# Kernel optimization log

Hardware: AMD Instinct MI355X
Metric: run time of the kernel (lower is better)

Reference implementation:

```python
import jax, jax.numpy as jnp
import numpy as np

V, T, E, H, B, S = 50000, 45, 256, 512, 32, 256


def setup_inputs() -> dict:
    key = jax.random.key(0)
    ks = jax.random.split(key, 14)
    s = 0.05
    return dict(
        x=jax.random.randint(ks[0], (B, S), 0, V),
        tags=jax.random.randint(ks[1], (B, S), 0, T),
        mask=jnp.ones((B, S), dtype=bool),
        emb=jax.random.normal(ks[2], (V, E), jnp.float32),
        Wih_f=jax.random.normal(ks[3], (4 * H, E), jnp.float32) * s,
        Whh_f=jax.random.normal(ks[4], (4 * H, H), jnp.float32) * s,
        bih_f=jnp.zeros((4 * H,), jnp.float32),
        bhh_f=jnp.zeros((4 * H,), jnp.float32),
        Wih_b=jax.random.normal(ks[5], (4 * H, E), jnp.float32) * s,
        Whh_b=jax.random.normal(ks[6], (4 * H, H), jnp.float32) * s,
        bih_b=jnp.zeros((4 * H,), jnp.float32),
        bhh_b=jnp.zeros((4 * H,), jnp.float32),
        Wout=jax.random.normal(ks[7], (T, 2 * H), jnp.float32) * s,
        bout=jnp.zeros((T,), jnp.float32),
        start=jax.random.normal(ks[8], (T,), jnp.float32) * 0.1,
        end=jax.random.normal(ks[9], (T,), jnp.float32) * 0.1,
        trans=jax.random.normal(ks[10], (T, T), jnp.float32) * 0.1,
    )


def _lstm_dir(xp, Whh, reverse):
    # xp: [S, B, 4H] precomputed input projection + biases; gate order i,f,g,o (torch)
    Bn = xp.shape[1]
    Hn = Whh.shape[1]
    def step(carry, g_in):
        h, c = carry
        g = g_in + h @ Whh.T
        i, f, gg, o = jnp.split(g, 4, axis=-1)
        c = jax.nn.sigmoid(f) * c + jax.nn.sigmoid(i) * jnp.tanh(gg)
        h = jax.nn.sigmoid(o) * jnp.tanh(c)
        return (h, c), h
    init = (jnp.zeros((Bn, Hn), xp.dtype), jnp.zeros((Bn, Hn), xp.dtype))
    _, hs = jax.lax.scan(step, init, xp, reverse=reverse)
    return hs  # [S, B, H]


def _crf_nll(emissions, tags, mask, start, end, trans):
    # emissions: [B, S, T]; neg mean log-likelihood (torchcrf, reduction='mean')
    mf = mask.astype(emissions.dtype)
    em_tag = jnp.take_along_axis(emissions, tags[:, :, None], axis=2)[:, :, 0]  # [B,S]
    num = start[tags[:, 0]] + em_tag[:, 0]
    num = num + ((trans[tags[:, :-1], tags[:, 1:]] + em_tag[:, 1:]) * mf[:, 1:]).sum(1)
    seq_ends = mf.sum(1).astype(tags.dtype) - 1
    last_tags = jnp.take_along_axis(tags, seq_ends[:, None], axis=1)[:, 0]
    num = num + end[last_tags]
    def denom_step(alpha, inp):
        em_t, m_t = inp  # [B,T], [B]
        nxt = jax.nn.logsumexp(alpha[:, :, None] + trans[None, :, :] + em_t[:, None, :], axis=1)
        return jnp.where(m_t[:, None] > 0, nxt, alpha), None
    alpha0 = start[None, :] + emissions[:, 0]
    em_rest = emissions.transpose(1, 0, 2)[1:]  # [S-1, B, T]
    alpha, _ = jax.lax.scan(denom_step, alpha0, (em_rest, mf.T[1:]))
    logZ = jax.nn.logsumexp(alpha + end[None, :], axis=1)
    return -(num - logZ).mean()


def reference(x, tags, mask, emb, Wih_f, Whh_f, bih_f, bhh_f,
              Wih_b, Whh_b, bih_b, bhh_b, Wout, bout, start, end, trans):
    embeds = emb[x]                      # [B, S, E]
    xs = embeds.transpose(1, 0, 2)       # [S, B, E]
    xp_f = jnp.einsum('sbe,ge->sbg', xs, Wih_f) + bih_f + bhh_f
    hs_f = _lstm_dir(xp_f, Whh_f, False)
    xp_b = jnp.einsum('sbe,ge->sbg', xs, Wih_b) + bih_b + bhh_b
    hs_b = _lstm_dir(xp_b, Whh_b, True)
    hcat = jnp.concatenate([hs_f, hs_b], axis=-1)          # [S, B, 2H]
    emissions = jnp.einsum('sbh,th->sbt', hcat, Wout) + bout
    emissions = emissions.transpose(1, 0, 2)                # [B, S, T]
    return _crf_nll(emissions, tags, mask, start, end, trans)
```

## Files before the change

### kernel.cpp

```cpp
#include <hip/hip_runtime.h>
#include <stdint.h>

#define S_LEN 256
#define B_N 32
#define H_N 512
#define E_N 256
#define T_N 45
#define G4H 2048

typedef unsigned short u16;
typedef unsigned int u32;
typedef u16 u16x8 __attribute__((ext_vector_type(8)));
typedef u16 u16x4 __attribute__((ext_vector_type(4)));
typedef u32 u32x4 __attribute__((ext_vector_type(4)));
typedef u32 u32x2 __attribute__((ext_vector_type(2)));
typedef __bf16 bf16x8 __attribute__((ext_vector_type(8)));
typedef float f32x4 __attribute__((ext_vector_type(4)));
typedef unsigned long long u64;

#define OFF_ATOK  256ull
#define OFF_WIHF  (OFF_ATOK + 4194304ull)
#define OFF_WIHB  (OFF_WIHF + 1048576ull)
#define OFF_WHHF  (OFF_WIHB + 1048576ull)
#define OFF_WHHB  (OFF_WHHF + 2097152ull)
#define OFF_WOUT  (OFF_WHHB + 2097152ull)
#define OFF_BSF   (OFF_WOUT + 98304ull)
#define OFF_BSB   (OFF_BSF + 8192ull)
#define OFF_XPF   (OFF_BSB + 8192ull)
#define OFF_XPB   (OFF_XPF + 33554432ull)
#define OFF_HSF   (OFF_XPB + 33554432ull)
#define OFF_HSB   (OFF_HSF + 8421376ull)
#define OFF_EM    (OFF_HSB + 8421376ull)

__device__ __forceinline__ u16 f2bf(float f) {
  union { float f; unsigned u; } v; v.f = f;
  unsigned r = v.u + 0x7FFFu + ((v.u >> 16) & 1u);
  return (u16)(r >> 16);
}
__device__ __forceinline__ float bf2f(u16 b) {
  union { unsigned u; float f; } v; v.u = ((unsigned)b) << 16;
  return v.f;
}
__device__ __forceinline__ bf16x8 ld8(const u16* p) {
  u16x8 v = *reinterpret_cast<const u16x8*>(p);
  return __builtin_bit_cast(bf16x8, v);
}
__device__ __forceinline__ void st_h8cc(u16* p, u16x4 v) {
  __hip_atomic_store(reinterpret_cast<u64*>(p), __builtin_bit_cast(u64, v),
                     __ATOMIC_RELAXED, __HIP_MEMORY_SCOPE_AGENT);
}
__device__ __forceinline__ u32x4 ld16cc(const u16* p) {
  u32x4 r;
  asm volatile("global_load_dwordx4 %0, %1, off sc1"
               : "=v"(r) : "v"(p) : "memory");
  return r;
}
__device__ __forceinline__ u32x2 ld8cc(const u16* p) {
  u32x2 r;
  asm volatile("global_load_dwordx2 %0, %1, off sc1"
               : "=v"(r) : "v"(p) : "memory");
  return r;
}
__device__ __forceinline__ void st2cc(u16* p, u32 v) {
  asm volatile("global_store_short %0, %1, off sc1"
               :: "v"(p), "v"(v) : "memory");
}
__device__ __forceinline__ f32x4 mfma16(bf16x8 a, bf16x8 b, f32x4 c) {
  return __builtin_amdgcn_mfma_f32_16x16x32_bf16(a, b, c, 0, 0, 0);
}
__device__ __forceinline__ float sigm(float x) { return 1.f / (1.f + __expf(-x)); }
__device__ __forceinline__ float tanhf_(float x) {
  float ax = fabsf(x);
  float e = __expf(-2.f * ax);
  float t = 1.f - 2.f * e / (1.f + e);
  return (x < 0.f) ? -t : t;
}
__device__ __forceinline__ float wredmax(float v) {
  #pragma unroll
  for (int m = 1; m < 64; m <<= 1) v = fmaxf(v, __shfl_xor(v, m));
  return v;
}
__device__ __forceinline__ float wredsum(float v) {
  #pragma unroll
  for (int m = 1; m < 64; m <<= 1) v += __shfl_xor(v, m);
  return v;
}

__global__ void k_castAW(const int* __restrict__ x, const float* __restrict__ emb,
                         u16* __restrict__ atok,
                         const float* __restrict__ WihF, const float* __restrict__ WihB,
                         const float* __restrict__ WhhF, const float* __restrict__ WhhB,
                         const float* __restrict__ Wout,
                         const float* __restrict__ bihF, const float* __restrict__ bhhF,
                         const float* __restrict__ bihB, const float* __restrict__ bhhB,
                         u16* wihf, u16* wihb, u16* whhf, u16* whhb, u16* woutp,
                         float* bsf, float* bsb, u16* hsf, u16* hsb) {
  int bid = blockIdx.x;
  if (bid < 1024) {
    int idx = bid * 256 + threadIdx.x;
    int t = idx >> 5;
    int e0 = (idx & 31) << 3;
    int s = t >> 5, b = t & 31;
    int xid = x[b * S_LEN + s];
    const float4* p = reinterpret_cast<const float4*>(emb + (size_t)xid * E_N + e0);
    float4 lo = p[0], hi = p[1];
    u16x8 o;
    o[0] = f2bf(lo.x); o[1] = f2bf(lo.y); o[2] = f2bf(lo.z); o[3] = f2bf(lo.w);
    o[4] = f2bf(hi.x); o[5] = f2bf(hi.y); o[6] = f2bf(hi.z); o[7] = f2bf(hi.w);
    *reinterpret_cast<u16x8*>(atok + (size_t)t * E_N + e0) = o;
    return;
  }
  int i = (bid - 1024) * 256 + threadIdx.x;
  if (i < 524288) { wihf[i] = f2bf(WihF[i]); return; }
  i -= 524288;
  if (i < 524288) { wihb[i] = f2bf(WihB[i]); return; }
  i -= 524288;
  if (i < 1048576) { whhf[i] = f2bf(WhhF[i]); return; }
  i -= 1048576;
  if (i < 1048576) { whhb[i] = f2bf(WhhB[i]); return; }
  i -= 1048576;
  if (i < 49152) {
    int n = i >> 10, k = i & 1023;
    woutp[i] = (n < T_N) ? f2bf(Wout[n * 1024 + k]) : (u16)0;
    return;
  }
  i -= 49152;
  if (i < 2048) { bsf[i] = bihF[i] + bhhF[i]; return; }
  i -= 2048;
  if (i < 2048) { bsb[i] = bihB[i] + bhhB[i]; return; }
  i -= 2048;
  if (i < 16384) { hsf[i] = 0; return; }
  i -= 16384;
  if (i < 16384) { hsb[(size_t)256 * 16384 + i] = 0; return; }
}

__global__ __launch_bounds__(128, 1) void k_fused(
    const u16* __restrict__ whhF, const u16* __restrict__ whhB,
    const u16* __restrict__ atok,
    const u16* __restrict__ wihF, const u16* __restrict__ wihB,
    const float* __restrict__ bsF, const float* __restrict__ bsB,
    u16* __restrict__ xpF, u16* __restrict__ xpB,
    u16* __restrict__ hsF, u16* __restrict__ hsB) {
  if (blockIdx.x >= 64) {
    int j = (int)blockIdx.x - 64;
    int dir = j & 1, idx = j >> 1;
    int tIdx = idx >> 4, gIdx = idx & 15;
    if (dir) tIdx = 127 - tIdx;
    const int wave = threadIdx.x >> 6, lane = threadIdx.x & 63;
    const int lr = lane & 15, lh = lane >> 4;
    const int t0 = tIdx * 64;
    const int g0 = gIdx * 128 + wave * 64;
    const u16* wih = dir ? wihB : wihF;
    const float* bs = dir ? bsB : bsF;
    u16* xp = dir ? xpB : xpF;
    f32x4 acc[4][4] = {};
    for (int kk = 0; kk < 8; ++kk) {
      int e = kk * 32 + lh * 8;
      bf16x8 a[4], bfr[4];
      #pragma unroll
      for (int mi = 0; mi < 4; ++mi) a[mi] = ld8(atok + (size_t)(t0 + 16 * mi + lr) * E_N + e);
      #pragma unroll
      for (int ni = 0; ni < 4; ++ni) bfr[ni] = ld8(wih + (size_t)(g0 + 16 * ni + lr) * E_N + e);
      #pragma unroll
      for (int mi = 0; mi < 4; ++mi)
        #pragma unroll
        for (int ni = 0; ni < 4; ++ni) acc[mi][ni] = mfma16(a[mi], bfr[ni], acc[mi][ni]);
    }
    #pragma unroll
    for (int ni = 0; ni < 4; ++ni) {
      int g = g0 + 16 * ni + lr;
      float bsv = bs[g];
      #pragma unroll
      for (int mi = 0; mi < 4; ++mi)
        #pragma unroll
        for (int r = 0; r < 4; ++r) {
          int t = t0 + 16 * mi + 4 * lh + r;
          st2cc(xp + (size_t)t * G4H + g, (u32)f2bf(acc[mi][ni][r] + bsv));
        }
    }
    return;
  }
  const int dir = blockIdx.x >> 5;
  const int w = blockIdx.x & 31;
  const int nt = threadIdx.x >> 6;
  const int lane = threadIdx.x & 63;
  const int lr = lane & 15, lh = lane >> 4;
  const u16* whh = dir ? whhB : whhF;
  const u16* xp = dir ? xpB : xpF;
  u16* hs = dir ? hsB : hsF;

  bf16x8 A[4][16];
  #pragma unroll
  for (int mt = 0; mt < 4; ++mt) {
    const u16* base = whh + (size_t)(mt * 512 + 16 * w + lr) * H_N + lh * 8;
    #pragma unroll
    for (int kk = 0; kk < 16; ++kk) A[mt][kk] = ld8(base + kk * 32);
  }
  const int b = nt * 16 + lr;
  const int j0 = 16 * w + 4 * lh;
  float cst[4] = {0.f, 0.f, 0.f, 0.f};

  for (int t = 0; t < S_LEN; ++t) {
    const int s = dir ? (S_LEN - 1 - t) : t;
    const int slot_r = dir ? (s + 1) : s;
    const int slot_w = dir ? s : (s + 1);

    u32x2 xqr[4];
    const u16* xpt = xp + ((size_t)(s * B_N + b)) * G4H + j0;
    #pragma unroll
    for (int mt = 0; mt < 4; ++mt) xqr[mt] = ld8cc(xpt + mt * 512);

    const u16* hp = hs + ((size_t)slot_r * B_N + b) * H_N + lh * 8;
    u32x4 raw[16];
    #pragma unroll
    for (int kk = 0; kk < 16; ++kk) raw[kk] = ld16cc(hp + kk * 32);
    asm volatile("s_waitcnt vmcnt(0)" ::: "memory");
    __builtin_amdgcn_sched_barrier(0);
    u32 pend = 0;
    #pragma unroll
    for (int kk = 0; kk < 16; ++kk)
      if (raw[kk][0] == 0xFFFFFFFFu || raw[kk][2] == 0xFFFFFFFFu) pend |= (1u << kk);
    while (__builtin_amdgcn_ballot_w64(pend != 0u)) {
      __builtin_amdgcn_s_sleep(1);
      #pragma unroll
      for (int kk = 0; kk < 16; ++kk)
        if (pend & (1u << kk)) raw[kk] = ld16cc(hp + kk * 32);
      asm volatile("s_waitcnt vmcnt(0)" ::: "memory");
      __builtin_amdgcn_sched_barrier(0);
      u32 np = 0;
      #pragma unroll
      for (int kk = 0; kk < 16; ++kk)
        if ((pend & (1u << kk)) &&
            (raw[kk][0] == 0xFFFFFFFFu || raw[kk][2] == 0xFFFFFFFFu)) np |= (1u << kk);
      pend = np;
    }

    f32x4 acc[4] = {};
    #pragma unroll
    for (int kk = 0; kk < 16; ++kk) {
      bf16x8 Bf = __builtin_bit_cast(bf16x8, raw[kk]);
      #pragma unroll
      for (int mt = 0; mt < 4; ++mt) acc[mt] = mfma16(A[mt][kk], Bf, acc[mt]);
    }

    for (;;) {
      u32 xbad = 0;
      #pragma unroll
      for (int mt = 0; mt < 4; ++mt) {
        #pragma unroll
        for (int d = 0; d < 2; ++d) {
          u32 wv = xqr[mt][d];
          xbad |= ((wv & 0xFFFFu) == 0xFFFFu) | ((wv >> 16) == 0xFFFFu);
        }
      }
      if (!__builtin_amdgcn_ballot_w64(xbad != 0u)) break;
      __builtin_amdgcn_s_sleep(1);
      #pragma unroll
      for (int mt = 0; mt < 4; ++mt) xqr[mt] = ld8cc(xpt + mt * 512);
      asm volatile("s_waitcnt vmcnt(0)" ::: "memory");
      __builtin_amdgcn_sched_barrier(0);
    }

    u16x4 hv;
    #pragma unroll
    for (int r = 0; r < 4; ++r) {
      u32 w0 = xqr[0][r >> 1], w1 = xqr[1][r >> 1], w2 = xqr[2][r >> 1], w3 = xqr[3][r >> 1];
      u16 x0 = (r & 1) ? (u16)(w0 >> 16) : (u16)(w0 & 0xFFFFu);
      u16 x1 = (r & 1) ? (u16)(w1 >> 16) : (u16)(w1 & 0xFFFFu);
      u16 x2 = (r & 1) ? (u16)(w2 >> 16) : (u16)(w2 & 0xFFFFu);
      u16 x3 = (r & 1) ? (u16)(w3 >> 16) : (u16)(w3 & 0xFFFFu);
      float gi = acc[0][r] + bf2f(x0);
      float gf = acc[1][r] + bf2f(x1);
      float gg = acc[2][r] + bf2f(x2);
      float go = acc[3][r] + bf2f(x3);
      float c = sigm(gf) * cst[r] + sigm(gi) * tanhf_(gg);
      cst[r] = c;
      hv[r] = f2bf(sigm(go) * tanhf_(c));
    }
    st_h8cc(hs + ((size_t)slot_w * B_N + b) * H_N + j0, hv);
  }
}

__global__ __launch_bounds__(256) void k_gemm_em(
    const u16* __restrict__ hsF, const u16* __restrict__ hsB,
    const u16* __restrict__ woutp, const float* __restrict__ bout, float* __restrict__ em) {
  const int wave = threadIdx.x >> 6, lane = threadIdx.x & 63;
  const int lr = lane & 15, lh = lane >> 4;
  const int t0 = blockIdx.x * 64 + wave * 16;
  f32x4 acc[3] = {};
  for (int kk = 0; kk < 32; ++kk) {
    int k = kk * 32 + lh * 8;
    int t = t0 + lr;
    int s = t >> 5, bt = t & 31;
    const u16* ap = (kk < 16) ? (hsF + ((size_t)(s + 1) * B_N + bt) * H_N + k)
                              : (hsB + ((size_t)s * B_N + bt) * H_N + (k - 512));
    bf16x8 a = ld8(ap);
    #pragma unroll
    for (int ni = 0; ni < 3; ++ni) {
      bf16x8 bb = ld8(woutp + (size_t)(16 * ni + lr) * 1024 + k);
      acc[ni] = mfma16(a, bb, acc[ni]);
    }
  }
  #pragma unroll
  for (int ni = 0; ni < 3; ++ni) {
    int tag = 16 * ni + lr;
    float bo = (tag < T_N) ? bout[tag] : 0.f;
    #pragma unroll
    for (int r = 0; r < 4; ++r) {
      int t = t0 + 4 * lh + r;
      em[(size_t)t * 48 + tag] = acc[ni][r] + bo;
    }
  }
}

__global__ __launch_bounds__(64) void k_crf(
    const float* __restrict__ em, const int* __restrict__ tags,
    const float* __restrict__ start, const float* __restrict__ endv,
    const float* __restrict__ trans, float* __restrict__ out) {
  __shared__ float tl[T_N * T_N + 32];
  const int b = blockIdx.x;
  const int lane = threadIdx.x;
  for (int i = lane; i < T_N * T_N + 32; i += 64)
    tl[i] = (i < T_N * T_N) ? trans[i] : 0.f;
  __syncthreads();
  float acur = (lane < T_N) ? (start[lane] + em[(size_t)b * 48 + lane]) : -1e30f;
  float emv_next = (lane < 48) ? em[((size_t)(1 * B_N + b)) * 48 + lane] : 0.f;
  for (int s = 1; s < S_LEN; ++s) {
    float shift = wredmax(acur);
    float emv = emv_next;
    if (s < S_LEN - 1)
      emv_next = (lane < 48) ? em[((size_t)((s + 1) * B_N + b)) * 48 + lane] : 0.f;
    float s0 = 0.f, s1 = 0.f, s2 = 0.f;
    #pragma unroll
    for (int t = 0; t < T_N; t += 3) {
      s0 += __expf(__shfl(acur, t)     + tl[t * T_N + lane]       - shift);
      s1 += __expf(__shfl(acur, t + 1) + tl[(t + 1) * T_N + lane] - shift);
      s2 += __expf(__shfl(acur, t + 2) + tl[(t + 2) * T_N + lane] - shift);
    }
    acur = (lane < T_N) ? (shift + __logf(s0 + s1 + s2) + emv) : -1e30f;
  }
  float z = (lane < T_N) ? (acur + endv[lane]) : -1e30f;
  float m = wredmax(z);
  float sum = wredsum((lane < T_N) ? __expf(z - m) : 0.f);
  float logZ = m + __logf(sum);
  float np = 0.f;
  #pragma unroll
  for (int q = 0; q < 4; ++q) {
    int s = 1 + lane * 4 + q;
    if (s < S_LEN) {
      int tp = tags[b * S_LEN + s - 1], tc = tags[b * S_LEN + s];
      np += tl[tp * T_N + tc] + em[((size_t)s * B_N + b) * 48 + tc];
    }
  }
  np = wredsum(np);
  if (lane == 0) {
    int tg0 = tags[b * S_LEN], tgL = tags[b * S_LEN + S_LEN - 1];
    float num = start[tg0] + em[(size_t)b * 48 + tg0] + np + endv[tgL];
    atomicAdd(out, -(num - logZ) / (float)B_N);
  }
}

extern "C" void kernel_launch(void* const* d_in, const int* in_sizes, int n_in,
                              void* d_out, int out_size, void* d_ws, size_t ws_size,
                              hipStream_t stream) {
  const int* x = (const int*)d_in[0];
  const int* tags = (const int*)d_in[1];
  const float* emb = (const float*)d_in[3];
  const float* WihF = (const float*)d_in[4];
  const float* WhhF = (const float*)d_in[5];
  const float* bihF = (const float*)d_in[6];
  const float* bhhF = (const float*)d_in[7];
  const float* WihB = (const float*)d_in[8];
  const float* WhhB = (const float*)d_in[9];
  const float* bihB = (const float*)d_in[10];
  const float* bhhB = (const float*)d_in[11];
  const float* Wout = (const float*)d_in[12];
  const float* bout = (const float*)d_in[13];
  const float* start = (const float*)d_in[14];
  const float* endv = (const float*)d_in[15];
  const float* trans = (const float*)d_in[16];
  float* out = (float*)d_out;
  char* ws = (char*)d_ws;

  u16* atok = (u16*)(ws + OFF_ATOK);
  u16* wihf = (u16*)(ws + OFF_WIHF);
  u16* wihb = (u16*)(ws + OFF_WIHB);
  u16* whhf = (u16*)(ws + OFF_WHHF);
  u16* whhb = (u16*)(ws + OFF_WHHB);
  u16* woutp = (u16*)(ws + OFF_WOUT);
  float* bsf = (float*)(ws + OFF_BSF);
  float* bsb = (float*)(ws + OFF_BSB);
  u16* xpf = (u16*)(ws + OFF_XPF);
  u16* xpb = (u16*)(ws + OFF_XPB);
  u16* hsf = (u16*)(ws + OFF_HSF);
  u16* hsb = (u16*)(ws + OFF_HSB);
  float* emis = (float*)(ws + OFF_EM);

  hipMemsetAsync(out, 0, sizeof(float), stream);
  hipMemsetAsync(ws + OFF_HSF + 32768ull, 0xFF, 16777216ull, stream);
  hipMemsetAsync(ws + OFF_XPF, 0xFF, 67108864ull, stream);
  k_castAW<<<13648, 256, 0, stream>>>(x, emb, atok, WihF, WihB, WhhF, WhhB, Wout,
                                      bihF, bhhF, bihB, bhhB,
                                      wihf, wihb, whhf, whhb, woutp, bsf, bsb, hsf, hsb);
  k_fused<<<4160, 128, 0, stream>>>(whhf, whhb, atok, wihf, wihb, bsf, bsb,
                                    xpf, xpb, hsf, hsb);
  k_gemm_em<<<128, 256, 0, stream>>>(hsf, hsb, woutp, bout, emis);
  k_crf<<<32, 64, 0, stream>>>(emis, tags, start, endv, trans, out);
}
```

Before: 1.501 ms.

## Fuse emission GEMM and CRF into persistent kernel via sentinel polling

Result: slower. 1.548 ms (+3.1%).

```diff
diff --git a/kernel.cpp b/kernel.cpp
--- a/kernel.cpp
+++ b/kernel.cpp
@@ -61,9 +61,19 @@
                : "=v"(r) : "v"(p) : "memory");
   return r;
 }
+__device__ __forceinline__ u32 ld4cc(const float* p) {
+  u32 r;
+  asm volatile("global_load_dword %0, %1, off sc1"
+               : "=v"(r) : "v"(p) : "memory");
+  return r;
+}
 __device__ __forceinline__ void st2cc(u16* p, u32 v) {
   asm volatile("global_store_short %0, %1, off sc1"
                :: "v"(p), "v"(v) : "memory");
+}
+__device__ __forceinline__ void st4cc(float* p, float v) {
+  asm volatile("global_store_dword %0, %1, off sc1"
+               :: "v"(p), "v"(__builtin_bit_cast(u32, v)) : "memory");
 }
 __device__ __forceinline__ f32x4 mfma16(bf16x8 a, bf16x8 b, f32x4 c) {
   return __builtin_amdgcn_mfma_f32_16x16x32_bf16(a, b, c, 0, 0, 0);
@@ -94,8 +104,23 @@
                          const float* __restrict__ bihF, const float* __restrict__ bhhF,
                          const float* __restrict__ bihB, const float* __restrict__ bhhB,
                          u16* wihf, u16* wihb, u16* whhf, u16* whhb, u16* woutp,
-                         float* bsf, float* bsb, u16* hsf, u16* hsb) {
+                         float* bsf, float* bsb, u16* hsf, u16* hsb,
+                         u16* hsfill, u16* xpfill, float* emfill, float* outp) {
   int bid = blockIdx.x;
+  if (bid >= 34512) { if (threadIdx.x == 0) *outp = 0.f; return; }
+  u32x4 sent = {0xFFFFFFFFu, 0xFFFFFFFFu, 0xFFFFFFFFu, 0xFFFFFFFFu};
+  if (bid >= 34128) {
+    reinterpret_cast<u32x4*>(emfill)[(size_t)(bid - 34128) * 256 + threadIdx.x] = sent;
+    return;
+  }
+  if (bid >= 17744) {
+    reinterpret_cast<u32x4*>(xpfill)[(size_t)(bid - 17744) * 256 + threadIdx.x] = sent;
+    return;
+  }
+  if (bid >= 13648) {
+    reinterpret_cast<u32x4*>(hsfill)[(size_t)(bid - 13648) * 256 + threadIdx.x] = sent;
+    return;
+  }
   if (bid < 1024) {
     int idx = bid * 256 + threadIdx.x;
     int t = idx >> 5;
@@ -140,9 +165,15 @@
     const u16* __restrict__ wihF, const u16* __restrict__ wihB,
     const float* __restrict__ bsF, const float* __restrict__ bsB,
     u16* __restrict__ xpF, u16* __restrict__ xpB,
-    u16* __restrict__ hsF, u16* __restrict__ hsB) {
-  if (blockIdx.x >= 64) {
-    int j = (int)blockIdx.x - 64;
+    u16* __restrict__ hsF, u16* __restrict__ hsB,
+    const u16* __restrict__ woutp, const float* __restrict__ bout,
+    float* __restrict__ em, const int* __restrict__ tags,
+    const float* __restrict__ startv, const float* __restrict__ endv,
+    const float* __restrict__ trans, float* __restrict__ out) {
+  __shared__ float tl[T_N * T_N + 64];
+  const int bid = (int)blockIdx.x;
+  if (bid >= 64 && bid < 4160) {
+    int j = bid - 64;
     int dir = j & 1, idx = j >> 1;
     int tIdx = idx >> 4, gIdx = idx & 15;
     if (dir) tIdx = 127 - tIdx;
@@ -180,8 +211,153 @@
     }
     return;
   }
-  const int dir = blockIdx.x >> 5;
-  const int w = blockIdx.x & 31;
+  if (bid >= 4160 && bid < 4416) {
+    const int s = bid - 4160;
+    const int wv = threadIdx.x >> 6, lane = threadIdx.x & 63;
+    const int lr = lane & 15, lh = lane >> 4;
+    const int b = wv * 16 + lr;
+    const u16* af = hsF + ((size_t)(s + 1) * B_N + b) * H_N + lh * 8;
+    const u16* ab = hsB + ((size_t)s * B_N + b) * H_N + lh * 8;
+    for (;;) {
+      u32x4 c0 = ld16cc(af);
+      u32x4 c1 = ld16cc(ab);
+      asm volatile("s_waitcnt vmcnt(0)" ::: "memory");
+      __builtin_amdgcn_sched_barrier(0);
+      u32 bad = (c0[0] == 0xFFFFFFFFu) | (c0[2] == 0xFFFFFFFFu) |
+                (c1[0] == 0xFFFFFFFFu) | (c1[2] == 0xFFFFFFFFu);
+      if (!__builtin_amdgcn_ballot_w64(bad != 0u)) break;
+      __builtin_amdgcn_s_sleep(32);
+    }
+    u32x4 raw[32];
+    #pragma unroll
+    for (int kk = 0; kk < 16; ++kk) raw[kk] = ld16cc(af + kk * 32);
+    #pragma unroll
+    for (int kk = 0; kk < 16; ++kk) raw[16 + kk] = ld16cc(ab + kk * 32);
+    asm volatile("s_waitcnt vmcnt(0)" ::: "memory");
+    __builtin_amdgcn_sched_barrier(0);
+    u32 pend = 0;
+    #pragma unroll
+    for (int kk = 0; kk < 32; ++kk)
+      if (raw[kk][0] == 0xFFFFFFFFu || raw[kk][2] == 0xFFFFFFFFu) pend |= (1u << kk);
+    while (__builtin_amdgcn_ballot_w64(pend != 0u)) {
+      __builtin_amdgcn_s_sleep(1);
+      #pragma unroll
+      for (int kk = 0; kk < 16; ++kk)
+        if (pend & (1u << kk)) raw[kk] = ld16cc(af + kk * 32);
+      #pragma unroll
+      for (int kk = 0; kk < 16; ++kk)
+        if (pend & (1u << (16 + kk))) raw[16 + kk] = ld16cc(ab + kk * 32);
+      asm volatile("s_waitcnt vmcnt(0)" ::: "memory");
+      __builtin_amdgcn_sched_barrier(0);
+      u32 np = 0;
+      #pragma unroll
+      for (int kk = 0; kk < 32; ++kk)
+        if ((pend & (1u << kk)) &&
+            (raw[kk][0] == 0xFFFFFFFFu || raw[kk][2] == 0xFFFFFFFFu)) np |= (1u << kk);
+      pend = np;
+    }
+    f32x4 acc[3] = {};
+    #pragma unroll
+    for (int kk = 0; kk < 32; ++kk) {
+      int k = kk * 32 + lh * 8;
+      bf16x8 a = __builtin_bit_cast(bf16x8, raw[kk]);
+      #pragma unroll
+      for (int ni = 0; ni < 3; ++ni) {
+        bf16x8 bb = ld8(woutp + (size_t)(16 * ni + lr) * 1024 + k);
+        acc[ni] = mfma16(a, bb, acc[ni]);
+      }
+    }
+    #pragma unroll
+    for (int ni = 0; ni < 3; ++ni) {
+      int tag = 16 * ni + lr;
+      float bo = (tag < T_N) ? bout[tag] : 0.f;
+      #pragma unroll
+      for (int r = 0; r < 4; ++r) {
+        int t = s * 32 + wv * 16 + 4 * lh + r;
+        st4cc(em + (size_t)t * 48 + tag, acc[ni][r] + bo);
+      }
+    }
+    return;
+  }
+  if (bid >= 4416) {
+    const int cb = bid - 4416;
+    const int wv = threadIdx.x >> 6, lane = threadIdx.x & 63;
+    const int b = cb * 2 + wv;
+    for (int i = threadIdx.x; i < T_N * T_N + 64; i += 128)
+      tl[i] = (i < T_N * T_N) ? trans[i] : 0.f;
+    __syncthreads();
+    u32 ev = 0u;
+    {
+      const float* row = em + (size_t)b * 48;
+      for (;;) {
+        if (lane < 48) ev = ld4cc(row + lane);
+        asm volatile("s_waitcnt vmcnt(0)" ::: "memory");
+        __builtin_amdgcn_sched_barrier(0);
+        if (!__builtin_amdgcn_ballot_w64(lane < 48 && ev == 0xFFFFFFFFu)) break;
+        __builtin_amdgcn_s_sleep(32);
+      }
+    }
+    float acur = (lane < T_N) ? (startv[lane] + __builtin_bit_cast(float, ev)) : -1e30f;
+    u32 evn = 0u;
+    if (lane < 48) evn = ld4cc(em + (size_t)(32 + b) * 48 + lane);
+    for (int s = 1; s < S_LEN; ++s) {
+      asm volatile("s_waitcnt vmcnt(0)" ::: "memory");
+      __builtin_amdgcn_sched_barrier(0);
+      while (__builtin_amdgcn_ballot_w64(lane < 48 && evn == 0xFFFFFFFFu)) {
+        __builtin_amdgcn_s_sleep(32);
+        if (lane < 48) evn = ld4cc(em + ((size_t)s * 32 + b) * 48 + lane);
+        asm volatile("s_waitcnt vmcnt(0)" ::: "memory");
+        __builtin_amdgcn_sched_barrier(0);
+      }
+      float emv = __builtin_bit_cast(float, evn);
+      if (s < S_LEN - 1 && lane < 48)
+        evn = ld4cc(em + ((size_t)(s + 1) * 32 + b) * 48 + lane);
+      float shift = wredmax(acur);
+      float s0 = 0.f, s1 = 0.f, s2 = 0.f;
+      #pragma unroll
+      for (int t = 0; t < T_N; t += 3) {
+        s0 += __expf(__shfl(acur, t)     + tl[t * T_N + lane]       - shift);
+        s1 += __expf(__shfl(acur, t + 1) + tl[(t + 1) * T_N + lane] - shift);
+        s2 += __expf(__shfl(acur, t + 2) + tl[(t + 2) * T_N + lane] - shift);
+      }
+      acur = (lane < T_N) ? (shift + __logf(s0 + s1 + s2) + emv) : -1e30f;
+    }
+    float z = (lane < T_N) ? (acur + endv[lane]) : -1e30f;
+    float m = wredmax(z);
+    float sum = wredsum((lane < T_N) ? __expf(z - m) : 0.f);
+    float logZ = m + __logf(sum);
+    u32 g[4]; float tlv[4];
+    #pragma unroll
+    for (int q = 0; q < 4; ++q) {
+      int s = 1 + lane * 4 + q;
+      g[q] = 0u; tlv[q] = 0.f;
+      if (s < S_LEN) {
+        int tp = tags[b * S_LEN + s - 1], tc = tags[b * S_LEN + s];
+        tlv[q] = tl[tp * T_N + tc];
+        g[q] = ld4cc(em + ((size_t)s * 32 + b) * 48 + tc);
+      }
+    }
+    asm volatile("s_waitcnt vmcnt(0)" ::: "memory");
+    __builtin_amdgcn_sched_barrier(0);
+    float np = 0.f;
+    #pragma unroll
+    for (int q = 0; q < 4; ++q) {
+      int s = 1 + lane * 4 + q;
+      if (s < S_LEN) np += tlv[q] + __builtin_bit_cast(float, g[q]);
+    }
+    np = wredsum(np);
+    if (lane == 0) {
+      int tg0 = tags[b * S_LEN], tgL = tags[b * S_LEN + S_LEN - 1];
+      u32 e0 = ld4cc(em + (size_t)b * 48 + tg0);
+      asm volatile("s_waitcnt vmcnt(0)" ::: "memory");
+      __builtin_amdgcn_sched_barrier(0);
+      float num = startv[tg0] + __builtin_bit_cast(float, e0) + np + endv[tgL];
+      atomicAdd(out, -(num - logZ) / (float)B_N);
+    }
+    return;
+  }
+  const int dir = bid >> 5;
+  const int w = bid & 31;
   const int nt = threadIdx.x >> 6;
   const int lane = threadIdx.x & 63;
   const int lr = lane & 15, lh = lane >> 4;
@@ -278,85 +454,6 @@
       hv[r] = f2bf(sigm(go) * tanhf_(c));
     }
     st_h8cc(hs + ((size_t)slot_w * B_N + b) * H_N + j0, hv);
-  }
-}
-
-__global__ __launch_bounds__(256) void k_gemm_em(
-    const u16* __restrict__ hsF, const u16* __restrict__ hsB,
-    const u16* __restrict__ woutp, const float* __restrict__ bout, float* __restrict__ em) {
-  const int wave = threadIdx.x >> 6, lane = threadIdx.x & 63;
-  const int lr = lane & 15, lh = lane >> 4;
-  const int t0 = blockIdx.x * 64 + wave * 16;
-  f32x4 acc[3] = {};
-  for (int kk = 0; kk < 32; ++kk) {
-    int k = kk * 32 + lh * 8;
-    int t = t0 + lr;
-    int s = t >> 5, bt = t & 31;
-    const u16* ap = (kk < 16) ? (hsF + ((size_t)(s + 1) * B_N + bt) * H_N + k)
-                              : (hsB + ((size_t)s * B_N + bt) * H_N + (k - 512));
-    bf16x8 a = ld8(ap);
-    #pragma unroll
-    for (int ni = 0; ni < 3; ++ni) {
-      bf16x8 bb = ld8(woutp + (size_t)(16 * ni + lr) * 1024 + k);
-      acc[ni] = mfma16(a, bb, acc[ni]);
-    }
-  }
-  #pragma unroll
-  for (int ni = 0; ni < 3; ++ni) {
-    int tag = 16 * ni + lr;
-    float bo = (tag < T_N) ? bout[tag] : 0.f;
-    #pragma unroll
-    for (int r = 0; r < 4; ++r) {
-      int t = t0 + 4 * lh + r;
-      em[(size_t)t * 48 + tag] = acc[ni][r] + bo;
-    }
-  }
-}
-
-__global__ __launch_bounds__(64) void k_crf(
-    const float* __restrict__ em, const int* __restrict__ tags,
-    const float* __restrict__ start, const float* __restrict__ endv,
-    const float* __restrict__ trans, float* __restrict__ out) {
-  __shared__ float tl[T_N * T_N + 32];
-  const int b = blockIdx.x;
-  const int lane = threadIdx.x;
-  for (int i = lane; i < T_N * T_N + 32; i += 64)
-    tl[i] = (i < T_N * T_N) ? trans[i] : 0.f;
-  __syncthreads();
-  float acur = (lane < T_N) ? (start[lane] + em[(size_t)b * 48 + lane]) : -1e30f;
-  float emv_next = (lane < 48) ? em[((size_t)(1 * B_N + b)) * 48 + lane] : 0.f;
-  for (int s = 1; s < S_LEN; ++s) {
-    float shift = wredmax(acur);
-    float emv = emv_next;
-    if (s < S_LEN - 1)
-      emv_next = (lane < 48) ? em[((size_t)((s + 1) * B_N + b)) * 48 + lane] : 0.f;
-    float s0 = 0.f, s1 = 0.f, s2 = 0.f;
-    #pragma unroll
-    for (int t = 0; t < T_N; t += 3) {
-      s0 += __expf(__shfl(acur, t)     + tl[t * T_N + lane]       - shift);
-      s1 += __expf(__shfl(acur, t + 1) + tl[(t + 1) * T_N + lane] - shift);
-      s2 += __expf(__shfl(acur, t + 2) + tl[(t + 2) * T_N + lane] - shift);
-    }
-    acur = (lane < T_N) ? (shift + __logf(s0 + s1 + s2) + emv) : -1e30f;
-  }
-  float z = (lane < T_N) ? (acur + endv[lane]) : -1e30f;
-  float m = wredmax(z);
-  float sum = wredsum((lane < T_N) ? __expf(z - m) : 0.f);
-  float logZ = m + __logf(sum);
-  float np = 0.f;
-  #pragma unroll
-  for (int q = 0; q < 4; ++q) {
-    int s = 1 + lane * 4 + q;
-    if (s < S_LEN) {
-      int tp = tags[b * S_LEN + s - 1], tc = tags[b * S_LEN + s];
-      np += tl[tp * T_N + tc] + em[((size_t)s * B_N + b) * 48 + tc];
-    }
-  }
-  np = wredsum(np);
-  if (lane == 0) {
-    int tg0 = tags[b * S_LEN], tgL = tags[b * S_LEN + S_LEN - 1];
-    float num = start[tg0] + em[(size_t)b * 48 + tg0] + np + endv[tgL];
-    atomicAdd(out, -(num - logZ) / (float)B_N);
   }
 }
 
@@ -376,7 +473,7 @@
   const float* bhhB = (const float*)d_in[11];
   const float* Wout = (const float*)d_in[12];
   const float* bout = (const float*)d_in[13];
-  const float* start = (const float*)d_in[14];
+  const float* startv = (const float*)d_in[14];
   const float* endv = (const float*)d_in[15];
   const float* trans = (const float*)d_in[16];
   float* out = (float*)d_out;
@@ -395,15 +492,13 @@
   u16* hsf = (u16*)(ws + OFF_HSF);
   u16* hsb = (u16*)(ws + OFF_HSB);
   float* emis = (float*)(ws + OFF_EM);
-
-  hipMemsetAsync(out, 0, sizeof(float), stream);
-  hipMemsetAsync(ws + OFF_HSF + 32768ull, 0xFF, 16777216ull, stream);
-  hipMemsetAsync(ws + OFF_XPF, 0xFF, 67108864ull, stream);
-  k_castAW<<<13648, 256, 0, stream>>>(x, emb, atok, WihF, WihB, WhhF, WhhB, Wout,
+  u16* hsfill = (u16*)(ws + OFF_HSF + 32768ull);
+
+  k_castAW<<<34513, 256, 0, stream>>>(x, emb, atok, WihF, WihB, WhhF, WhhB, Wout,
                                       bihF, bhhF, bihB, bhhB,
-                                      wihf, wihb, whhf, whhb, woutp, bsf, bsb, hsf, hsb);
-  k_fused<<<4160, 128, 0, stream>>>(whhf, whhb, atok, wihf, wihb, bsf, bsb,
-                                    xpf, xpb, hsf, hsb);
-  k_gemm_em<<<128, 256, 0, stream>>>(hsf, hsb, woutp, bout, emis);
-  k_crf<<<32, 64, 0, stream>>>(emis, tags, start, endv, trans, out);
-}
+                                      wihf, wihb, whhf, whhb, woutp, bsf, bsb, hsf, hsb,
+                                      hsfill, xpf, emis, out);
+  k_fused<<<4432, 128, 0, stream>>>(whhf, whhb, atok, wihf, wihb, bsf, bsb,
+                                    xpf, xpb, hsf, hsb,
+                                    woutp, bout, emis, tags, startv, endv, trans, out);
+}
```
